# Optimization experiments

Hardware: AMD Instinct MI355X
Metric: run time of the kernel (lower is better)

The kernel has to match this reference:

```python
import jax, jax.numpy as jnp
import numpy as np

PI_2 = 3.14159 / 2  # matches the torch module's pi_2 constant
EPS = 1e-8          # F.cosine_similarity default eps


def setup_inputs() -> dict:
    key = jax.random.key(0)
    k1, k2 = jax.random.split(key)
    B, N, C, H, W = 32, 2000, 512, 7, 7
    key_t = jax.random.normal(k1, (B, C, H, W), dtype=jnp.float32)
    memory = jax.random.normal(k2, (N, C, H, W), dtype=jnp.float32)
    return {"key": key_t, "memory": memory}


def reference(key, memory):
    # Memory.read(key): cosine-similarity addressing + tan warp + softmax, then weighted read.
    B = key.shape[0]
    N = memory.shape[0]
    k = key.reshape(B, -1)        # [B, D], D = C*H*W
    m = memory.reshape(N, -1)     # [N, D]
    # cosine similarity with torch's eps clamping on norms
    dots = jnp.einsum('bd,nd->bn', k, m)                                   # [B, N]
    k_norm = jnp.maximum(jnp.sqrt(jnp.sum(k * k, axis=-1, keepdims=True)), EPS)  # [B, 1]
    m_norm = jnp.maximum(jnp.sqrt(jnp.sum(m * m, axis=-1)), EPS)                 # [N]
    cos = dots / (k_norm * m_norm[None, :])                                 # [B, N]
    w = jax.nn.softmax(jnp.tan(cos * PI_2), axis=1)                         # [B, N]
    # weighted read: sum_n w[b,n] * memory[n,c,h,w] -> [B, C, H, W]
    out = jnp.einsum('bn,nchw->bchw', w, memory)
    return out
```

## Files before the change

kernel.cpp:

```cpp
#include <hip/hip_runtime.h>
#include <math.h>

#define D_ELEMS 25088
#define D4      6272
#define D2      12544
#define N_MEM   2000
#define B_KEYS  32
#define PI_2F   1.570795f
#define EPSF    1e-8f


__global__ __launch_bounds__(256) void k_zero(float* __restrict__ ws) {
    ws[blockIdx.x * 256 + threadIdx.x] = 0.f;
}

__global__ __launch_bounds__(256) void k_dots(const float* __restrict__ key,
                                              const float* __restrict__ mem,
                                              float* __restrict__ dots,
                                              float* __restrict__ mnorm2) {
    const int nb   = blockIdx.x >> 1;
    const int s    = blockIdx.x & 1;
    const int n0   = nb * 8;
    const int bg   = threadIdx.x >> 6;
    const int lane = threadIdx.x & 63;

    const float4* K4 = (const float4*)key;
    const float4* M4 = (const float4*)mem;

    float acc[8][8];
#pragma unroll
    for (int j = 0; j < 8; ++j)
#pragma unroll
        for (int i = 0; i < 8; ++i) acc[j][i] = 0.f;
    float msq[8] = {0.f,0.f,0.f,0.f,0.f,0.f,0.f,0.f};

    const int c0 = s * 49;
    for (int c = 0; c < 49; ++c) {
        const int d4 = (c0 + c) * 64 + lane;
        float4 kf[8], mf[8];
#pragma unroll
        for (int i = 0; i < 8; ++i) kf[i] = K4[(bg * 8 + i) * D4 + d4];
#pragma unroll
        for (int j = 0; j < 8; ++j) mf[j] = M4[(n0 + j) * D4 + d4];
#pragma unroll
        for (int j = 0; j < 8; ++j) {
#pragma unroll
            for (int i = 0; i < 8; ++i) {
                acc[j][i] += mf[j].x * kf[i].x + mf[j].y * kf[i].y
                           + mf[j].z * kf[i].z + mf[j].w * kf[i].w;
            }
        }
        if (bg == 0) {
#pragma unroll
            for (int j = 0; j < 8; ++j)
                msq[j] += mf[j].x * mf[j].x + mf[j].y * mf[j].y
                        + mf[j].z * mf[j].z + mf[j].w * mf[j].w;
        }
    }

#pragma unroll
    for (int off = 8; off < 64; off <<= 1)
#pragma unroll
        for (int j = 0; j < 8; ++j)
#pragma unroll
            for (int i = 0; i < 8; ++i)
                acc[j][i] += __shfl_xor(acc[j][i], off, 64);

    __shared__ float red[4][8][65];
    if (lane < 8) {
#pragma unroll
        for (int j = 0; j < 8; ++j)
#pragma unroll
            for (int i = 0; i < 8; ++i)
                red[bg][lane][j * 8 + i] = acc[j][i];
    }
    __syncthreads();

    float ssum = red[bg][0][lane];
#pragma unroll
    for (int i = 1; i < 8; ++i) ssum += red[bg][i][lane];
    atomicAdd(&dots[(n0 + (lane >> 3)) * B_KEYS + bg * 8 + (lane & 7)], ssum);

    if (bg == 0) {
#pragma unroll
        for (int off = 1; off < 64; off <<= 1)
#pragma unroll
            for (int j = 0; j < 8; ++j)
                msq[j] += __shfl_xor(msq[j], off, 64);
        if (lane == 0) {
#pragma unroll
            for (int j = 0; j < 8; ++j) atomicAdd(&mnorm2[n0 + j], msq[j]);
        }
    }
}

__global__ __launch_bounds__(256) void k_softmax(const float* __restrict__ key,
                                                 const float* __restrict__ dots,
                                                 const float* __restrict__ mnorm2,
                                                 float* __restrict__ w) {
    const int b   = blockIdx.x;
    const int tid = threadIdx.x;
    __shared__ float sred[256];
    __shared__ float xbuf[N_MEM];

    const float4* K4 = (const float4*)(key + (size_t)b * D_ELEMS);
    float ks = 0.f;
    for (int i = tid; i < D4; i += 256) {
        float4 kf = K4[i];
        ks += kf.x * kf.x + kf.y * kf.y + kf.z * kf.z + kf.w * kf.w;
    }
    sred[tid] = ks;
    __syncthreads();
    for (int o = 128; o; o >>= 1) {
        if (tid < o) sred[tid] += sred[tid + o];
        __syncthreads();
    }
    const float knorm = fmaxf(sqrtf(sred[0]), EPSF);
    __syncthreads();

    float mx = -1e30f;
    for (int n = tid; n < N_MEM; n += 256) {
        float mn   = fmaxf(sqrtf(mnorm2[n]), EPSF);
        float cosv = dots[n * B_KEYS + b] / (knorm * mn);
        float x    = tanf(cosv * PI_2F);
        xbuf[n] = x;
        mx = fmaxf(mx, x);
    }
    sred[tid] = mx;
    __syncthreads();
    for (int o = 128; o; o >>= 1) {
        if (tid < o) sred[tid] = fmaxf(sred[tid], sred[tid + o]);
        __syncthreads();
    }
    mx = sred[0];
    __syncthreads();

    float sm = 0.f;
    for (int n = tid; n < N_MEM; n += 256) sm += expf(xbuf[n] - mx);
    sred[tid] = sm;
    __syncthreads();
    for (int o = 128; o; o >>= 1) {
        if (tid < o) sred[tid] += sred[tid + o];
        __syncthreads();
    }
    const float inv = 1.f / sred[0];
    __syncthreads();

    for (int n = tid; n < N_MEM; n += 256)
        w[n * B_KEYS + b] = expf(xbuf[n] - mx) * inv;
}

__global__ __launch_bounds__(128) void k_read(const float* __restrict__ mem,
                                              const float* __restrict__ w,
                                              float* __restrict__ partial,
                                              int nPerS) {
    const int db = blockIdx.x % 98;
    const int s  = blockIdx.x / 98;
    const int n0 = s * nPerS;
    const int d2 = db * 128 + threadIdx.x;

    const float2* M2 = (const float2*)mem;
    __shared__ float wls[128 * B_KEYS];

    float accx[B_KEYS], accy[B_KEYS];
#pragma unroll
    for (int b = 0; b < B_KEYS; ++b) { accx[b] = 0.f; accy[b] = 0.f; }

    for (int t0 = 0; t0 < nPerS; t0 += 128) {
        const int tn = min(128, nPerS - t0);
        __syncthreads();
        for (int i = threadIdx.x; i < tn * B_KEYS; i += 128)
            wls[i] = w[(n0 + t0) * B_KEYS + i];
        __syncthreads();
        for (int nn = 0; nn < tn; ++nn) {
            const float2 mv = M2[(size_t)(n0 + t0 + nn) * D2 + d2];
            const float* wn = wls + nn * B_KEYS;
#pragma unroll
            for (int b = 0; b < B_KEYS; ++b) {
                const float wv = wn[b];
                accx[b] += wv * mv.x;
                accy[b] += wv * mv.y;
            }
        }
    }

    float2* P2 = (float2*)partial;
#pragma unroll
    for (int b = 0; b < B_KEYS; ++b)
        P2[(size_t)(s * B_KEYS + b) * D2 + d2] = make_float2(accx[b], accy[b]);
}

__global__ __launch_bounds__(256) void k_finish(const float* __restrict__ partial,
                                                float* __restrict__ out, int ns) {
    const int i = blockIdx.x * 256 + threadIdx.x;
    float sum = 0.f;
    for (int s = 0; s < ns; ++s) sum += partial[(size_t)s * (B_KEYS * D_ELEMS) + i];
    out[i] = sum;
}

extern "C" void kernel_launch(void* const* d_in, const int* in_sizes, int n_in,
                              void* d_out, int out_size, void* d_ws, size_t ws_size,
                              hipStream_t stream) {
    (void)in_sizes; (void)n_in; (void)out_size;
    const float* key = (const float*)d_in[0];
    const float* mem = (const float*)d_in[1];
    float* out = (float*)d_out;
    float* ws  = (float*)d_ws;

    float* dots   = ws;
    float* mnorm2 = ws + 64000;
    float* part   = ws + 66048;

    int ns = 16;
    while (ns > 1 && (size_t)(66048 + (size_t)ns * 802816) * 4 > ws_size) ns >>= 1;
    const int nPerS = N_MEM / ns;

    k_zero   <<<258, 256, 0, stream>>>(ws);
    k_dots   <<<500, 256, 0, stream>>>(key, mem, dots, mnorm2);
    k_softmax<<<B_KEYS, 256, 0, stream>>>(key, dots, mnorm2, dots);
    k_read   <<<98 * ns, 128, 0, stream>>>(mem, dots, part, nPerS);
    k_finish <<<3136, 256, 0, stream>>>(part, out, ns);
}
```

Baseline: 409.4 us.

## Split read kernel across key groups and raise dots kernel parallelism

```diff
diff --git a/kernel.cpp b/kernel.cpp
--- a/kernel.cpp
+++ b/kernel.cpp
@@ -18,8 +18,8 @@
                                               const float* __restrict__ mem,
                                               float* __restrict__ dots,
                                               float* __restrict__ mnorm2) {
-    const int nb   = blockIdx.x >> 1;
-    const int s    = blockIdx.x & 1;
+    const int nb   = blockIdx.x / 7;
+    const int s    = blockIdx.x % 7;
     const int n0   = nb * 8;
     const int bg   = threadIdx.x >> 6;
     const int lane = threadIdx.x & 63;
@@ -34,8 +34,8 @@
         for (int i = 0; i < 8; ++i) acc[j][i] = 0.f;
     float msq[8] = {0.f,0.f,0.f,0.f,0.f,0.f,0.f,0.f};
 
-    const int c0 = s * 49;
-    for (int c = 0; c < 49; ++c) {
+    const int c0 = s * 14;
+    for (int c = 0; c < 14; ++c) {
         const int d4 = (c0 + c) * 64 + lane;
         float4 kf[8], mf[8];
 #pragma unroll
@@ -150,44 +150,41 @@
         w[n * B_KEYS + b] = expf(xbuf[n] - mx) * inv;
 }
 
-__global__ __launch_bounds__(128) void k_read(const float* __restrict__ mem,
+__global__ __launch_bounds__(512) void k_read(const float* __restrict__ mem,
                                               const float* __restrict__ w,
                                               float* __restrict__ partial,
                                               int nPerS) {
-    const int db = blockIdx.x % 98;
-    const int s  = blockIdx.x / 98;
-    const int n0 = s * nPerS;
-    const int d2 = db * 128 + threadIdx.x;
+    const int db   = blockIdx.x % 98;
+    const int s    = blockIdx.x / 98;
+    const int n0   = s * nPerS;
+    const int bgrp = threadIdx.x >> 7;
+    const int b0   = bgrp * 8;
+    const int d2   = db * 128 + (threadIdx.x & 127);
 
     const float2* M2 = (const float2*)mem;
-    __shared__ float wls[128 * B_KEYS];
-
-    float accx[B_KEYS], accy[B_KEYS];
-#pragma unroll
-    for (int b = 0; b < B_KEYS; ++b) { accx[b] = 0.f; accy[b] = 0.f; }
-
-    for (int t0 = 0; t0 < nPerS; t0 += 128) {
-        const int tn = min(128, nPerS - t0);
-        __syncthreads();
-        for (int i = threadIdx.x; i < tn * B_KEYS; i += 128)
-            wls[i] = w[(n0 + t0) * B_KEYS + i];
-        __syncthreads();
-        for (int nn = 0; nn < tn; ++nn) {
-            const float2 mv = M2[(size_t)(n0 + t0 + nn) * D2 + d2];
-            const float* wn = wls + nn * B_KEYS;
-#pragma unroll
-            for (int b = 0; b < B_KEYS; ++b) {
-                const float wv = wn[b];
-                accx[b] += wv * mv.x;
-                accy[b] += wv * mv.y;
-            }
+    const float4* W4 = (const float4*)w;
+
+    float accx[8], accy[8];
+#pragma unroll
+    for (int i = 0; i < 8; ++i) { accx[i] = 0.f; accy[i] = 0.f; }
+
+    for (int nn = 0; nn < nPerS; ++nn) {
+        const int n = n0 + nn;
+        const float2 mv = M2[(size_t)n * D2 + d2];
+        const float4 wa = W4[n * 8 + bgrp * 2];
+        const float4 wb = W4[n * 8 + bgrp * 2 + 1];
+        const float wv[8] = {wa.x, wa.y, wa.z, wa.w, wb.x, wb.y, wb.z, wb.w};
+#pragma unroll
+        for (int i = 0; i < 8; ++i) {
+            accx[i] += wv[i] * mv.x;
+            accy[i] += wv[i] * mv.y;
         }
     }
 
     float2* P2 = (float2*)partial;
 #pragma unroll
-    for (int b = 0; b < B_KEYS; ++b)
-        P2[(size_t)(s * B_KEYS + b) * D2 + d2] = make_float2(accx[b], accy[b]);
+    for (int i = 0; i < 8; ++i)
+        P2[(size_t)(s * B_KEYS + b0 + i) * D2 + d2] = make_float2(accx[i], accy[i]);
 }
 
 __global__ __launch_bounds__(256) void k_finish(const float* __restrict__ partial,
@@ -216,8 +213,8 @@
     const int nPerS = N_MEM / ns;
 
     k_zero   <<<258, 256, 0, stream>>>(ws);
-    k_dots   <<<500, 256, 0, stream>>>(key, mem, dots, mnorm2);
+    k_dots   <<<1750, 256, 0, stream>>>(key, mem, dots, mnorm2);
     k_softmax<<<B_KEYS, 256, 0, stream>>>(key, dots, mnorm2, dots);
-    k_read   <<<98 * ns, 128, 0, stream>>>(mem, dots, part, nPerS);
+    k_read   <<<98 * ns, 512, 0, stream>>>(mem, dots, part, nPerS);
     k_finish <<<3136, 256, 0, stream>>>(part, out, ns);
 }
```

New measurement: 520.2 us. 27.1% more time.
